# Kernel optimization log

Hardware: AMD Instinct MI355X
Metric: run time of the kernel (lower is better)

Reference implementation:

```python
import jax, jax.numpy as jnp
import numpy as np

N_NODES = 50000
N_EDGES = 600000
IN_DIM = 128


def _glorot(key, shape, fan_in, fan_out):
    lim = float(np.sqrt(6.0 / (fan_in + fan_out)))
    return jax.random.uniform(key, shape, jnp.float32, -lim, lim)


def setup_inputs() -> dict:
    key = jax.random.key(0)
    ks = jax.random.split(key, 16)
    x = jax.random.normal(ks[0], (N_NODES, IN_DIM), jnp.float32)
    src = jax.random.randint(ks[1], (N_EDGES,), 0, N_NODES)
    off = jax.random.randint(ks[2], (N_EDGES,), 1, N_NODES)
    dst = (src + off) % N_NODES  # guarantees src != dst
    edge_index = jnp.stack([src, dst]).astype(jnp.int64)
    weights = jax.random.normal(ks[3], (N_EDGES,), jnp.float32)
    # layer 1: GATv2Conv(128, 64, heads=2) -> out 128 (concat)
    Wl1 = _glorot(ks[4], (128, 128), 128, 128)
    bl1 = jnp.zeros((128,), jnp.float32)
    Wr1 = _glorot(ks[5], (128, 128), 128, 128)
    br1 = jnp.zeros((128,), jnp.float32)
    att1 = _glorot(ks[6], (2, 64), 64, 64)
    bias1 = jnp.zeros((128,), jnp.float32)
    # layer 2: GATv2Conv(128, 4, heads=1, concat=False)
    Wl2 = _glorot(ks[7], (128, 4), 128, 4)
    bl2 = jnp.zeros((4,), jnp.float32)
    Wr2 = _glorot(ks[8], (128, 4), 128, 4)
    br2 = jnp.zeros((4,), jnp.float32)
    att2 = _glorot(ks[9], (1, 4), 4, 4)
    bias2 = jnp.zeros((4,), jnp.float32)
    return dict(x=x, edge_index=edge_index, weights=weights,
                Wl1=Wl1, bl1=bl1, Wr1=Wr1, br1=br1, att1=att1, bias1=bias1,
                Wl2=Wl2, bl2=bl2, Wr2=Wr2, br2=br2, att2=att2, bias2=bias2)


def gatv2_layer(x, src, dst, Wl, bl, Wr, br, att, bias, heads, ch, concat):
    # PyG GATv2Conv, eval mode (attention dropout off).
    N = x.shape[0]
    xl = (x @ Wl + bl).reshape(N, heads, ch)  # source transform (messages)
    xr = (x @ Wr + br).reshape(N, heads, ch)  # target transform
    e = xl[src] + xr[dst]                     # [E, H, C]
    e = jnp.where(e > 0, e, 0.2 * e)          # leaky_relu, negative_slope=0.2
    alpha = jnp.einsum('ehc,hc->eh', e, att)  # [E, H]
    amax = jax.ops.segment_max(alpha, dst, num_segments=N)
    amax = jnp.where(jnp.isfinite(amax), amax, 0.0)
    ex = jnp.exp(alpha - amax[dst])
    denom = jax.ops.segment_sum(ex, dst, num_segments=N)
    a = ex / (denom[dst] + 1e-16)             # segment softmax over in-edges
    out = jax.ops.segment_sum(a[:, :, None] * xl[src], dst, num_segments=N)
    out = out.reshape(N, heads * ch) if concat else out.mean(axis=1)
    return out + bias


def reference(x, edge_index, weights,
              Wl1, bl1, Wr1, br1, att1, bias1,
              Wl2, bl2, Wr2, br2, att2, bias2):
    N = x.shape[0]
    loop = jnp.arange(N, dtype=edge_index.dtype)
    src = jnp.concatenate([edge_index[0], loop])  # add self loops
    dst = jnp.concatenate([edge_index[1], loop])
    h = gatv2_layer(x, src, dst, Wl1, bl1, Wr1, br1, att1, bias1,
                    heads=2, ch=64, concat=True)
    h = jnp.where(h > 0, h, 0.01 * h)  # nn.LeakyReLU default slope 0.01
    h = gatv2_layer(h, src, dst, Wl2, bl2, Wr2, br2, att2, bias2,
                    heads=1, ch=4, concat=False)
    return jax.nn.softmax(h, axis=1)
```

## Files before the change

### kernel.cpp

```cpp
#include <hip/hip_runtime.h>

#define N_NODES 50000
#define N_EDGES 600000
#define E_TOT   650000
#define EBLK    2540
#define GBLK    391
#define ZBLK    196
#define MAXD    64

typedef __attribute__((ext_vector_type(8))) short short8;
typedef __attribute__((ext_vector_type(4))) float f32x4;

__device__ inline short f2bf(float f) {
  union { float f; unsigned u; } v; v.f = f;
  unsigned r = (v.u + 0x7FFFu + ((v.u >> 16) & 1u)) >> 16;
  return (short)r;
}
__device__ inline float bf2f(short u) {
  union { unsigned u; float f; } v; v.u = ((unsigned)(unsigned short)u) << 16;
  return v.f;
}


__global__ __launch_bounds__(256) void init_kernel(
    int* __restrict__ deg,
    const float* __restrict__ Wl, const float* __restrict__ Wr, short* __restrict__ Wbf) {
  int b = blockIdx.x;
  if (b < ZBLK) {
    int i = b * 256 + threadIdx.x;
    if (i < N_NODES) deg[i] = 0;
  } else {
    int gid = (b - ZBLK) * 256 + threadIdx.x;
    int c = gid >> 4, k8 = (gid & 15) * 8;
    const float* W = (c < 128) ? Wl : Wr;
    int cc = c & 127;
    short8 o;
    #pragma unroll
    for (int j = 0; j < 8; ++j) o[j] = f2bf(W[(size_t)(k8 + j) * 128 + cc]);
    *(short8*)(Wbf + (size_t)c * 128 + k8) = o;
  }
}


#define LSWZ(row, k) (((row) * 128 + (k)) ^ (((row) & 7) << 3))

__global__ __launch_bounds__(256) void gemm_build(
    const float* __restrict__ x, const short* __restrict__ Wbf,
    const float* __restrict__ bl, const float* __restrict__ br,
    short* __restrict__ xl, short* __restrict__ xr,
    const int* __restrict__ ei, int* __restrict__ deg, int* __restrict__ ell) {
  __shared__ short As[128 * 128];
  __shared__ short Bs[128 * 128];
  int t = threadIdx.x;

  if (blockIdx.x >= GBLK) {
    int e = (blockIdx.x - GBLK) * 256 + t;
    if (e < E_TOT) {
      int s, d;
      if (e < N_EDGES) { s = ei[e]; d = ei[N_EDGES + e]; }
      else             { s = e - N_EDGES; d = s; }
      int pos = atomicAdd(&deg[d], 1);
      ell[d * MAXD + pos] = s;
    }
    return;
  }

  int row0 = blockIdx.x * 128;

  #pragma unroll
  for (int i = 0; i < 8; ++i) {
    int c = t + 256 * i;
    int r = c >> 4, k8 = (c & 15) * 8;
    int gr = row0 + r;
    short8 o = {};
    if (gr < N_NODES) {
      const float* p = x + (size_t)gr * 128 + k8;
      f32x4 a = *(const f32x4*)p, b = *(const f32x4*)(p + 4);
      o[0] = f2bf(a.x); o[1] = f2bf(a.y); o[2] = f2bf(a.z); o[3] = f2bf(a.w);
      o[4] = f2bf(b.x); o[5] = f2bf(b.y); o[6] = f2bf(b.z); o[7] = f2bf(b.w);
    }
    *(short8*)(&As[LSWZ(r, k8)]) = o;
  }

  int w = t >> 6, lane = t & 63;
  int wm = (w >> 1) * 64, wn = (w & 1) * 64;
  int lr = lane & 15, lk = (lane >> 4) * 8;

  for (int hb = 0; hb < 2; ++hb) {
    #pragma unroll
    for (int i = 0; i < 8; ++i) {
      int c = t + 256 * i;
      int col = c >> 4, k8 = (c & 15) * 8;
      short8 o = *(const short8*)(Wbf + (size_t)(hb * 128 + col) * 128 + k8);
      *(short8*)(&Bs[LSWZ(col, k8)]) = o;
    }
    __syncthreads();

    f32x4 acc[4][4];
    #pragma unroll
    for (int m = 0; m < 4; ++m)
      #pragma unroll
      for (int n = 0; n < 4; ++n) acc[m][n] = (f32x4){0.f, 0.f, 0.f, 0.f};

    #pragma unroll
    for (int ks = 0; ks < 4; ++ks) {
      int k0 = ks * 32 + lk;
      short8 af[4], bfr[4];
      #pragma unroll
      for (int m = 0; m < 4; ++m) {
        int r = wm + m * 16 + lr;
        af[m] = *(const short8*)(&As[LSWZ(r, k0)]);
      }
      #pragma unroll
      for (int n = 0; n < 4; ++n) {
        int r = wn + n * 16 + lr;
        bfr[n] = *(const short8*)(&Bs[LSWZ(r, k0)]);
      }
      #pragma unroll
      for (int m = 0; m < 4; ++m)
        #pragma unroll
        for (int n = 0; n < 4; ++n)
          acc[m][n] = __builtin_amdgcn_mfma_f32_16x16x32_bf16(af[m], bfr[n], acc[m][n], 0, 0, 0);
    }

    const float* B0 = hb ? br : bl;
    short* O = hb ? xr : xl;
    int orow = (lane >> 4) * 4;
    #pragma unroll
    for (int n = 0; n < 4; ++n) {
      int col = wn + n * 16 + lr;
      float bv = B0[col];
      #pragma unroll
      for (int m = 0; m < 4; ++m) {
        #pragma unroll
        for (int r = 0; r < 4; ++r) {
          int grow = row0 + wm + m * 16 + orow + r;
          if (grow < N_NODES) O[(size_t)grow * 128 + col] = f2bf(acc[m][n][r] + bv);
        }
      }
    }
    __syncthreads();
  }
}


__global__ __launch_bounds__(256) void agg1_fused(
    const short* __restrict__ xl1, const short* __restrict__ xr1,
    const float* __restrict__ att, const float* __restrict__ bias,
    const float* __restrict__ Wl2, const float* __restrict__ bl2,
    const float* __restrict__ Wr2, const float* __restrict__ br2,
    const int* __restrict__ deg, const int* __restrict__ ell,
    float* __restrict__ xl2, float* __restrict__ xr2) {
  __shared__ short sbuf[4][8][512];
  int gid = blockIdx.x * 256 + threadIdx.x;
  int node = gid >> 4;
  int t = threadIdx.x;
  int wid = t >> 6, lane = t & 63;
  int L = lane & 15;
  int gbase = lane & 48;

  short8 xr8 = *(const short8*)(xr1 + (size_t)node * 128 + L * 8);
  float xr[8], at[8];
  #pragma unroll
  for (int r = 0; r < 8; ++r) xr[r] = bf2f(xr8[r]);
  *(float4*)(at)     = *(const float4*)(att + L * 8);
  *(float4*)(at + 4) = *(const float4*)(att + L * 8 + 4);

  float m = -1e30f, denom = 0.f;
  float acc[8];
  #pragma unroll
  for (int r = 0; r < 8; ++r) acc[r] = 0.f;

  int p1 = deg[node];
  const int* erow = ell + (size_t)node * MAXD;

  for (int base = 0; base < p1; base += 8) {
    int pE = base + L;
    int myidx = erow[pE < p1 ? pE : p1 - 1];
    #pragma unroll
    for (int j = 0; j < 8; ++j) {
      int ij = __shfl(myidx, gbase + j);
      const short* gp = xl1 + (size_t)ij * 128 + L * 8;
      __builtin_amdgcn_global_load_lds(
          (const __attribute__((address_space(1))) void*)gp,
          (__attribute__((address_space(3))) void*)&sbuf[wid][j][0],
          16, 0, 0);
    }
    asm volatile("s_waitcnt vmcnt(0)" ::: "memory");
    __builtin_amdgcn_sched_barrier(0);

    float pa[8];
    #pragma unroll
    for (int j = 0; j < 8; ++j) {
      short8 v = *(const short8*)(&sbuf[wid][j][lane * 8]);
      float s = 0.f;
      #pragma unroll
      for (int r = 0; r < 8; ++r) {
        float e = bf2f(v[r]) + xr[r];
        e = fmaxf(e, 0.2f * e);
        s = fmaf(e, at[r], s);
      }
      pa[j] = s;
    }
    #pragma unroll
    for (int st = 1; st < 8; st <<= 1) {
      #pragma unroll
      for (int j = 0; j < 8; ++j) pa[j] += __shfl_xor(pa[j], st);
    }
    #pragma unroll
    for (int j = 0; j < 8; ++j) pa[j] = (base + j < p1) ? pa[j] : -1e30f;
    float bm = pa[0];
    #pragma unroll
    for (int j = 1; j < 8; ++j) bm = fmaxf(bm, pa[j]);
    float mnew  = fmaxf(m, bm);
    float scale = __expf(m - mnew);
    float wgt[8], dsum = 0.f;
    #pragma unroll
    for (int j = 0; j < 8; ++j) { wgt[j] = __expf(pa[j] - mnew); dsum += wgt[j]; }
    denom = denom * scale + dsum;
    #pragma unroll
    for (int r = 0; r < 8; ++r) acc[r] *= scale;
    #pragma unroll
    for (int j = 0; j < 8; ++j) {
      short8 v = *(const short8*)(&sbuf[wid][j][lane * 8]);
      #pragma unroll
      for (int r = 0; r < 8; ++r) acc[r] = fmaf(wgt[j], bf2f(v[r]), acc[r]);
    }
    m = mnew;
  }

  float inv = 1.f / (denom + 1e-16f);
  float o[8];
  #pragma unroll
  for (int r = 0; r < 8; ++r) {
    float v = acc[r] * inv + bias[L * 8 + r];
    o[r] = fmaxf(v, 0.01f * v);
  }
  float pl[4] = {0.f, 0.f, 0.f, 0.f}, pr[4] = {0.f, 0.f, 0.f, 0.f};
  #pragma unroll
  for (int r = 0; r < 8; ++r) {
    float4 wl = *(const float4*)(Wl2 + (size_t)(L * 8 + r) * 4);
    float4 wr = *(const float4*)(Wr2 + (size_t)(L * 8 + r) * 4);
    pl[0] += o[r] * wl.x;  pl[1] += o[r] * wl.y;  pl[2] += o[r] * wl.z;  pl[3] += o[r] * wl.w;
    pr[0] += o[r] * wr.x;  pr[1] += o[r] * wr.y;  pr[2] += o[r] * wr.z;  pr[3] += o[r] * wr.w;
  }
  #pragma unroll
  for (int off = 1; off < 16; off <<= 1) {
    #pragma unroll
    for (int c = 0; c < 4; ++c) {
      pl[c] += __shfl_xor(pl[c], off);
      pr[c] += __shfl_xor(pr[c], off);
    }
  }
  if (L == 0) {
    float4 b0 = *(const float4*)(bl2);
    float4 b1 = *(const float4*)(br2);
    *(float4*)(xl2 + (size_t)node * 4) =
        make_float4(pl[0] + b0.x, pl[1] + b0.y, pl[2] + b0.z, pl[3] + b0.w);
    *(float4*)(xr2 + (size_t)node * 4) =
        make_float4(pr[0] + b1.x, pr[1] + b1.y, pr[2] + b1.z, pr[3] + b1.w);
  }
}


__global__ __launch_bounds__(256) void agg2_kernel(
    const float* __restrict__ xl2, const float* __restrict__ xr2,
    const float* __restrict__ att, const float* __restrict__ bias,
    const int* __restrict__ deg, const int* __restrict__ ell,
    float* __restrict__ out) {
  int gid = blockIdx.x * 256 + threadIdx.x;
  int node = gid >> 4;
  if (node >= N_NODES) return;
  int L = threadIdx.x & 15;
  float4 xr = *(const float4*)(xr2 + (size_t)node * 4);
  float4 at = *(const float4*)(att);
  float m = -1e30f, denom = 0.f;
  float4 acc = make_float4(0.f, 0.f, 0.f, 0.f);
  int p1 = deg[node];
  const int* erow = ell + (size_t)node * MAXD;
  int nit = (p1 + 15) >> 4;
  int p = L;
  for (int it = 0; it < nit; ++it) {
    bool valid = p < p1;
    int s = erow[valid ? p : p1 - 1];
    float4 xv = *(const float4*)(xl2 + (size_t)s * 4);
    float e0 = xv.x + xr.x; e0 = fmaxf(e0, 0.2f * e0);
    float e1 = xv.y + xr.y; e1 = fmaxf(e1, 0.2f * e1);
    float e2 = xv.z + xr.z; e2 = fmaxf(e2, 0.2f * e2);
    float e3 = xv.w + xr.w; e3 = fmaxf(e3, 0.2f * e3);
    float pa = e0 * at.x + e1 * at.y + e2 * at.z + e3 * at.w;
    pa = valid ? pa : -1e30f;
    float mnew  = fmaxf(m, pa);
    float scale = __expf(m - mnew);
    float wgt   = __expf(pa - mnew);
    denom = denom * scale + wgt;
    acc.x = acc.x * scale + wgt * xv.x;
    acc.y = acc.y * scale + wgt * xv.y;
    acc.z = acc.z * scale + wgt * xv.z;
    acc.w = acc.w * scale + wgt * xv.w;
    m = mnew;
    p += 16;
  }
  #pragma unroll
  for (int off = 1; off < 16; off <<= 1) {
    float mo = __shfl_xor(m, off);
    float dn = __shfl_xor(denom, off);
    float ax = __shfl_xor(acc.x, off);
    float ay = __shfl_xor(acc.y, off);
    float az = __shfl_xor(acc.z, off);
    float aw = __shfl_xor(acc.w, off);
    float mnew = fmaxf(m, mo);
    float sa = __expf(m - mnew);
    float sb = __expf(mo - mnew);
    denom = denom * sa + dn * sb;
    acc.x = acc.x * sa + ax * sb;
    acc.y = acc.y * sa + ay * sb;
    acc.z = acc.z * sa + az * sb;
    acc.w = acc.w * sa + aw * sb;
    m = mnew;
  }
  if (L == 0) {
    float inv = 1.f / (denom + 1e-16f);
    float4 b = *(const float4*)(bias);
    float o0 = acc.x * inv + b.x;
    float o1 = acc.y * inv + b.y;
    float o2 = acc.z * inv + b.z;
    float o3 = acc.w * inv + b.w;
    float mx = fmaxf(fmaxf(o0, o1), fmaxf(o2, o3));
    float q0 = __expf(o0 - mx), q1 = __expf(o1 - mx), q2 = __expf(o2 - mx), q3 = __expf(o3 - mx);
    float r = 1.f / (q0 + q1 + q2 + q3);
    *(float4*)(out + (size_t)node * 4) = make_float4(q0 * r, q1 * r, q2 * r, q3 * r);
  }
}


extern "C" void kernel_launch(void* const* d_in, const int* in_sizes, int n_in,
                              void* d_out, int out_size, void* d_ws, size_t ws_size,
                              hipStream_t stream) {
  (void)in_sizes; (void)n_in; (void)out_size; (void)ws_size;
  const float* x     = (const float*)d_in[0];
  const int*   ei    = (const int*)d_in[1];
  const float* Wl1   = (const float*)d_in[3];
  const float* bl1   = (const float*)d_in[4];
  const float* Wr1   = (const float*)d_in[5];
  const float* br1   = (const float*)d_in[6];
  const float* att1  = (const float*)d_in[7];
  const float* bias1 = (const float*)d_in[8];
  const float* Wl2   = (const float*)d_in[9];
  const float* bl2   = (const float*)d_in[10];
  const float* Wr2   = (const float*)d_in[11];
  const float* br2   = (const float*)d_in[12];
  const float* att2  = (const float*)d_in[13];
  const float* bias2 = (const float*)d_in[14];
  float* out = (float*)d_out;

  char* w = (char*)d_ws;
  auto alloc = [&](size_t bytes) -> char* {
    char* p = w;
    w += (bytes + 255) & ~(size_t)255;
    return p;
  };
  short* xl1    = (short*)alloc((size_t)N_NODES * 128 * 2);
  short* xr1    = (short*)alloc((size_t)N_NODES * 128 * 2);
  float* xl2    = (float*)alloc((size_t)N_NODES * 4 * 4);
  float* xr2    = (float*)alloc((size_t)N_NODES * 4 * 4);
  int*   deg    = (int*)alloc((size_t)N_NODES * 4);
  int*   ell    = (int*)alloc((size_t)N_NODES * MAXD * 4);
  short* Wbf    = (short*)alloc((size_t)256 * 128 * 2);

  init_kernel<<<ZBLK + 16, 256, 0, stream>>>(deg, Wl1, Wr1, Wbf);
  gemm_build<<<GBLK + EBLK, 256, 0, stream>>>(x, Wbf, bl1, br1, xl1, xr1, ei, deg, ell);
  agg1_fused<<<(N_NODES * 16 + 255) / 256, 256, 0, stream>>>(
      xl1, xr1, att1, bias1, Wl2, bl2, Wr2, br2, deg, ell, xl2, xr2);
  agg2_kernel<<<(N_NODES * 16 + 255) / 256, 256, 0, stream>>>(
      xl2, xr2, att2, bias2, deg, ell, out);
}
```

Before: 128.2 us.

## Load GEMM operands directly into registers, dropping LDS staging and barriers

The node-feature GEMM no longer stages the x tile and the bf16 weights in shared memory. Each wave loads its A fragments straight from global memory into registers, converting to bf16 on the fly, and reads B fragments directly from global Wbf. This removes 64 KB of LDS per block and all __syncthreads, which should raise occupancy and cut barrier stalls. In exchange, A rows are fetched redundantly by the two waves that share a row range, B is fetched by every block from global/L2 with less coalesced 16-byte accesses, and the register count rises (16 short8 A fragments per thread).

```diff
diff --git a/kernel.cpp b/kernel.cpp
--- a/kernel.cpp
+++ b/kernel.cpp
@@ -42,15 +42,11 @@
 }
 
 
-#define LSWZ(row, k) (((row) * 128 + (k)) ^ (((row) & 7) << 3))
-
 __global__ __launch_bounds__(256) void gemm_build(
     const float* __restrict__ x, const short* __restrict__ Wbf,
     const float* __restrict__ bl, const float* __restrict__ br,
     short* __restrict__ xl, short* __restrict__ xr,
     const int* __restrict__ ei, int* __restrict__ deg, int* __restrict__ ell) {
-  __shared__ short As[128 * 128];
-  __shared__ short Bs[128 * 128];
   int t = threadIdx.x;
 
   if (blockIdx.x >= GBLK) {
@@ -66,36 +62,28 @@
   }
 
   int row0 = blockIdx.x * 128;
-
-  #pragma unroll
-  for (int i = 0; i < 8; ++i) {
-    int c = t + 256 * i;
-    int r = c >> 4, k8 = (c & 15) * 8;
-    int gr = row0 + r;
-    short8 o = {};
-    if (gr < N_NODES) {
-      const float* p = x + (size_t)gr * 128 + k8;
-      f32x4 a = *(const f32x4*)p, b = *(const f32x4*)(p + 4);
-      o[0] = f2bf(a.x); o[1] = f2bf(a.y); o[2] = f2bf(a.z); o[3] = f2bf(a.w);
-      o[4] = f2bf(b.x); o[5] = f2bf(b.y); o[6] = f2bf(b.z); o[7] = f2bf(b.w);
-    }
-    *(short8*)(&As[LSWZ(r, k8)]) = o;
-  }
-
   int w = t >> 6, lane = t & 63;
   int wm = (w >> 1) * 64, wn = (w & 1) * 64;
   int lr = lane & 15, lk = (lane >> 4) * 8;
 
+  short8 af[4][4];
+  #pragma unroll
+  for (int ks = 0; ks < 4; ++ks) {
+    #pragma unroll
+    for (int m = 0; m < 4; ++m) {
+      int gr = row0 + wm + m * 16 + lr;
+      gr = gr < N_NODES ? gr : N_NODES - 1;
+      const float* p = x + (size_t)gr * 128 + ks * 32 + lk;
+      f32x4 a = *(const f32x4*)p, b = *(const f32x4*)(p + 4);
+      short8 o;
+      o[0] = f2bf(a.x); o[1] = f2bf(a.y); o[2] = f2bf(a.z); o[3] = f2bf(a.w);
+      o[4] = f2bf(b.x); o[5] = f2bf(b.y); o[6] = f2bf(b.z); o[7] = f2bf(b.w);
+      af[ks][m] = o;
+    }
+  }
+
+  #pragma unroll
   for (int hb = 0; hb < 2; ++hb) {
-    #pragma unroll
-    for (int i = 0; i < 8; ++i) {
-      int c = t + 256 * i;
-      int col = c >> 4, k8 = (c & 15) * 8;
-      short8 o = *(const short8*)(Wbf + (size_t)(hb * 128 + col) * 128 + k8);
-      *(short8*)(&Bs[LSWZ(col, k8)]) = o;
-    }
-    __syncthreads();
-
     f32x4 acc[4][4];
     #pragma unroll
     for (int m = 0; m < 4; ++m)
@@ -104,23 +92,17 @@
 
     #pragma unroll
     for (int ks = 0; ks < 4; ++ks) {
-      int k0 = ks * 32 + lk;
-      short8 af[4], bfr[4];
-      #pragma unroll
-      for (int m = 0; m < 4; ++m) {
-        int r = wm + m * 16 + lr;
-        af[m] = *(const short8*)(&As[LSWZ(r, k0)]);
-      }
+      short8 bfr[4];
       #pragma unroll
       for (int n = 0; n < 4; ++n) {
-        int r = wn + n * 16 + lr;
-        bfr[n] = *(const short8*)(&Bs[LSWZ(r, k0)]);
+        int col = hb * 128 + wn + n * 16 + lr;
+        bfr[n] = *(const short8*)(Wbf + (size_t)col * 128 + ks * 32 + lk);
       }
       #pragma unroll
       for (int m = 0; m < 4; ++m)
         #pragma unroll
         for (int n = 0; n < 4; ++n)
-          acc[m][n] = __builtin_amdgcn_mfma_f32_16x16x32_bf16(af[m], bfr[n], acc[m][n], 0, 0, 0);
+          acc[m][n] = __builtin_amdgcn_mfma_f32_16x16x32_bf16(af[ks][m], bfr[n], acc[m][n], 0, 0, 0);
     }
 
     const float* B0 = hb ? br : bl;
@@ -139,7 +121,6 @@
         }
       }
     }
-    __syncthreads();
   }
 }
 
```

Result: faster. 124.5 us (-2.8%).
